# Kernel tuning notes

Hardware: AMD Instinct MI355X
Metric: run time of the kernel (lower is better)

Reference implementation:

```python
import jax, jax.numpy as jnp
import numpy as np

N = 65536        # nodes
E = 131072       # directed edges
D = 512          # emb_dim
L = 5            # num_layer
G = 512          # num graphs
EPS = 1e-5       # batchnorm eps
NUM_ATOM_TYPE, NUM_CHIRALITY = 120, 3
NUM_BOND_TYPE, NUM_BOND_DIR = 6, 3


def setup_inputs() -> dict:
    key = jax.random.key(0)
    ks = jax.random.split(key, 12)
    s = 0.02
    return {
        "x": jax.random.randint(ks[0], (N, 2), 0, 3),
        "edge_index": jax.random.randint(ks[1], (2, E), 0, N),
        "edge_attr": jax.random.randint(ks[2], (E, 2), 0, 3),
        "batch": jnp.sort(jax.random.randint(ks[3], (N,), 0, G)),
        "x_emb1": jax.random.normal(ks[4], (NUM_ATOM_TYPE, D), jnp.float32) * s,
        "x_emb2": jax.random.normal(ks[5], (NUM_CHIRALITY, D), jnp.float32) * s,
        "e_emb1": jax.random.normal(ks[6], (L, NUM_BOND_TYPE, D), jnp.float32) * s,
        "e_emb2": jax.random.normal(ks[7], (L, NUM_BOND_DIR, D), jnp.float32) * s,
        "W1": jax.random.normal(ks[8], (L, D, 2 * D), jnp.float32) * s,
        "b1": jnp.zeros((L, 2 * D), jnp.float32),
        "W2": jax.random.normal(ks[9], (L, 2 * D, D), jnp.float32) * s,
        "b2": jnp.zeros((L, D), jnp.float32),
        "gamma": jnp.ones((L, D), jnp.float32),
        "beta": jnp.zeros((L, D), jnp.float32),
    }


def reference(x, edge_index, edge_attr, batch,
              x_emb1, x_emb2, e_emb1, e_emb2,
              W1, b1, W2, b2, gamma, beta):
    n = x.shape[0]
    # atom embedding: type + chirality
    h = x_emb1[x[:, 0]] + x_emb2[x[:, 1]]                     # [N, D]

    # add self loops (appended after real edges, attr = [4, 0])
    loops = jnp.arange(n)
    src = jnp.concatenate([edge_index[0], loops])             # [E+N]
    dst = jnp.concatenate([edge_index[1], loops])
    sl_attr = jnp.concatenate(
        [jnp.full((n, 1), 4, dtype=edge_attr.dtype),
         jnp.zeros((n, 1), dtype=edge_attr.dtype)], axis=1)
    ea = jnp.concatenate([edge_attr, sl_attr], axis=0)        # [E+N, 2]

    for l in range(L):
        # per-edge embedding: bond type + bond direction
        e = e_emb1[l][ea[:, 0]] + e_emb2[l][ea[:, 1]]         # [E+N, D]
        msg = h[src] + e                                      # gather + add
        agg = jax.ops.segment_sum(msg, dst, num_segments=n)   # scatter-add
        # GIN MLP: Linear(D,2D) -> ReLU -> Linear(2D,D)
        hh = jax.nn.relu(agg @ W1[l] + b1[l]) @ W2[l] + b2[l]
        # BatchNorm1d (training-mode batch statistics)
        mean = hh.mean(axis=0)
        var = hh.var(axis=0)
        hh = (hh - mean) * jax.lax.rsqrt(var + EPS) * gamma[l] + beta[l]
        if l < L - 1:
            hh = jax.nn.relu(hh)   # dropout(p=0) is identity
        h = hh

    # JK='last': node rep = h; graph rep = global mean pool over batch ids
    counts = jax.ops.segment_sum(jnp.ones((n,), h.dtype), batch, num_segments=G)
    graph = jax.ops.segment_sum(h, batch, num_segments=G) / jnp.maximum(counts, 1.0)[:, None]
    return graph, h
```

## Files before the change

kernel.cpp:

```cpp
#include <hip/hip_runtime.h>
#include <stdint.h>

#define Nn 65536
#define Ee 131072
#define Dd 512
#define D2 1024
#define Ll 5
#define Gg 512
#define EPSf 1e-5f

typedef _Float16 f16x8 __attribute__((ext_vector_type(8)));
typedef float f32x4 __attribute__((ext_vector_type(4)));
typedef unsigned short u16x8 __attribute__((ext_vector_type(8)));

__device__ __forceinline__ unsigned short f2h(float f) {
    _Float16 h = (_Float16)f;
    union { _Float16 h; unsigned short u; } c; c.h = h;
    return c.u;
}

__device__ __forceinline__ float h2f(unsigned short s) {
    union { unsigned short s; _Float16 h; } c; c.s = s;
    return (float)c.h;
}

__device__ __forceinline__ void gload_lds16(const void* g, void* l) {
    __builtin_amdgcn_global_load_lds(
        (const __attribute__((address_space(1))) void*)(uintptr_t)g,
        (__attribute__((address_space(3))) void*)(unsigned)(uintptr_t)l,
        16, 0, 0);
}

__global__ void k_transW(const float* __restrict__ src, unsigned short* __restrict__ dst,
                         int K, int Nw) {
    long total = (long)Ll * K * Nw;
    for (long idx = (long)blockIdx.x * blockDim.x + threadIdx.x; idx < total;
         idx += (long)gridDim.x * blockDim.x) {
        long l = idx / ((long)K * Nw);
        long rem = idx - l * (long)K * Nw;
        int k = (int)(rem / Nw), n = (int)(rem % Nw);
        dst[(l * Nw + n) * K + k] = f2h(src[idx]);
    }
}

__global__ void k_etab(const float* __restrict__ ee1, const float* __restrict__ ee2,
                       float* __restrict__ E) {
    int idx = blockIdx.x * blockDim.x + threadIdx.x;
    const int total = Ll * 18 * Dd;
    if (idx < total) {
        int l = idx / (18 * Dd);
        int rem = idx - l * 18 * Dd;
        int j = rem / Dd, c = rem - j * Dd;
        int a0 = j / 3, a1 = j - a0 * 3;
        E[idx] = ee1[((size_t)l * 6 + a0) * Dd + c] + ee2[((size_t)l * 3 + a1) * Dd + c];
    }
}

__global__ void k_embed(const int* __restrict__ x,
                        const float* __restrict__ xe1, const float* __restrict__ xe2,
                        unsigned short* __restrict__ hhf) {
    const int total = Nn * 64;
    for (int idx = blockIdx.x * blockDim.x + threadIdx.x; idx < total;
         idx += gridDim.x * blockDim.x) {
        int node = idx >> 6, c8 = (idx & 63) * 8;
        int t0 = x[2 * node], t1 = x[2 * node + 1];
        const float4* p1 = (const float4*)(xe1 + (size_t)t0 * Dd + c8);
        const float4* p2 = (const float4*)(xe2 + (size_t)t1 * Dd + c8);
        float4 a0 = p1[0], a1 = p1[1], b0 = p2[0], b1 = p2[1];
        u16x8 o;
        o[0] = f2h(a0.x + b0.x); o[1] = f2h(a0.y + b0.y);
        o[2] = f2h(a0.z + b0.z); o[3] = f2h(a0.w + b0.w);
        o[4] = f2h(a1.x + b1.x); o[5] = f2h(a1.y + b1.y);
        o[6] = f2h(a1.z + b1.z); o[7] = f2h(a1.w + b1.w);
        *(u16x8*)(hhf + (size_t)node * Dd + c8) = o;
    }
}

__global__ void k_zeroN(int* __restrict__ p, int n) {
    int i = blockIdx.x * blockDim.x + threadIdx.x;
    if (i < n) p[i] = 0;
}

__global__ void k_hist(const int* __restrict__ edst, int* __restrict__ cnt) {
    int e = blockIdx.x * blockDim.x + threadIdx.x;
    if (e < Ee) atomicAdd(&cnt[edst[e]], 1);
}

__global__ void k_scan(const int* __restrict__ cnt, int* __restrict__ off,
                       int* __restrict__ cursor) {
    __shared__ int part[1024];
    int t = threadIdx.x;
    int base = t * 64;
    int s = 0;
    for (int i = 0; i < 64; ++i) s += cnt[base + i];
    part[t] = s;
    __syncthreads();
    for (int d = 1; d < 1024; d <<= 1) {
        int v = (t >= d) ? part[t - d] : 0;
        __syncthreads();
        part[t] += v;
        __syncthreads();
    }
    int run = part[t] - s;
    for (int i = 0; i < 64; ++i) {
        off[base + i] = run;
        cursor[base + i] = run;
        run += cnt[base + i];
    }
    if (t == 1023) off[Nn] = run;
}

__global__ void k_place(const int* __restrict__ esrc, const int* __restrict__ edst,
                        const int* __restrict__ eattr, int* __restrict__ cursor,
                        int* __restrict__ ckey, int* __restrict__ csrc) {
    int e = blockIdx.x * blockDim.x + threadIdx.x;
    if (e < Ee) {
        int d = edst[e];
        int p = atomicAdd(&cursor[d], 1);
        ckey[p] = e * 32 + (eattr[2 * e] * 3 + eattr[2 * e + 1]);
        csrc[p] = esrc[e];
    }
}

__global__ void k_sort(const int* __restrict__ off, int* __restrict__ ckey,
                       int* __restrict__ csrc) {
    int node = blockIdx.x * blockDim.x + threadIdx.x;
    if (node >= Nn) return;
    int kb = off[node], ke = off[node + 1];
    for (int i = kb + 1; i < ke; ++i) {
        int k = ckey[i], s = csrc[i];
        int j = i - 1;
        while (j >= kb && ckey[j] > k) {
            ckey[j + 1] = ckey[j]; csrc[j + 1] = csrc[j]; --j;
        }
        ckey[j + 1] = k; csrc[j + 1] = s;
    }
}

template <int NORM>
__global__ __launch_bounds__(256) void k_gather(const unsigned short* __restrict__ hf16,
                                                const float* __restrict__ ss,
                                                const int* __restrict__ off,
                                                const int* __restrict__ ckey,
                                                const int* __restrict__ csrc,
                                                const float* __restrict__ El,
                                                unsigned short* __restrict__ aggh) {
    int node = (blockIdx.x << 2) + (threadIdx.x >> 6);
    int lane = threadIdx.x & 63;
    int c8 = lane * 8;
    float sa[8], sb[8];
    if (NORM) {
        float4 a0 = *(const float4*)(ss + c8), a1 = *(const float4*)(ss + c8 + 4);
        float4 b0 = *(const float4*)(ss + 512 + c8), b1 = *(const float4*)(ss + 512 + c8 + 4);
        sa[0] = a0.x; sa[1] = a0.y; sa[2] = a0.z; sa[3] = a0.w;
        sa[4] = a1.x; sa[5] = a1.y; sa[6] = a1.z; sa[7] = a1.w;
        sb[0] = b0.x; sb[1] = b0.y; sb[2] = b0.z; sb[3] = b0.w;
        sb[4] = b1.x; sb[5] = b1.y; sb[6] = b1.z; sb[7] = b1.w;
    }
    float acc[8];
    {
        u16x8 v = *(const u16x8*)(hf16 + (size_t)node * Dd + c8);
        float4 e0 = *(const float4*)(El + 12 * Dd + c8);
        float4 e1 = *(const float4*)(El + 12 * Dd + c8 + 4);
        float ev[8];
        ev[0] = e0.x; ev[1] = e0.y; ev[2] = e0.z; ev[3] = e0.w;
        ev[4] = e1.x; ev[5] = e1.y; ev[6] = e1.z; ev[7] = e1.w;
#pragma unroll
        for (int i = 0; i < 8; ++i) {
            float hv = h2f(v[i]);
            if (NORM) hv = fmaxf(fmaf(hv, sa[i], sb[i]), 0.f);
            acc[i] = hv + ev[i];
        }
    }
    int kb = off[node], ke = off[node + 1];
    for (int k = kb; k < ke; ++k) {
        int src = csrc[k];
        int at = ckey[k] & 31;
        u16x8 v = *(const u16x8*)(hf16 + (size_t)src * Dd + c8);
        const float* Er = El + (size_t)at * Dd + c8;
        float4 e0 = *(const float4*)(Er);
        float4 e1 = *(const float4*)(Er + 4);
        float ev[8];
        ev[0] = e0.x; ev[1] = e0.y; ev[2] = e0.z; ev[3] = e0.w;
        ev[4] = e1.x; ev[5] = e1.y; ev[6] = e1.z; ev[7] = e1.w;
#pragma unroll
        for (int i = 0; i < 8; ++i) {
            float hv = h2f(v[i]);
            if (NORM) hv = fmaxf(fmaf(hv, sa[i], sb[i]), 0.f);
            acc[i] += hv + ev[i];
        }
    }
    u16x8 o;
#pragma unroll
    for (int i = 0; i < 8; ++i) o[i] = f2h(acc[i]);
    *(u16x8*)(aggh + (size_t)node * Dd + c8) = o;
}

__device__ __forceinline__ void stage_q(const unsigned short* __restrict__ g, int ldk,
                                        long row0, int col0, char* region, int tid) {
    int wbase = (tid >> 6) << 10;
#pragma unroll
    for (int r = 0; r < 2; ++r) {
        int gi = tid + r * 512;
        int row = gi >> 2;
        int k16 = (gi & 3) ^ ((row >> 1) & 3);
        gload_lds16(g + (row0 + row) * (long)ldk + col0 + k16 * 8,
                    region + r * 8192 + wbase);
    }
}

__device__ __forceinline__ f16x8 rd_frag(const char* region, int row, int l4) {
    int slot = l4 ^ ((row >> 1) & 3);
    return *(const f16x8*)(region + row * 64 + (slot << 4));
}

template <int EPI>
__global__ __launch_bounds__(512, 2) void gemm8(const unsigned short* __restrict__ A,
                                                const unsigned short* __restrict__ BT,
                                                const float* __restrict__ bias,
                                                unsigned short* __restrict__ Cb,
                                                float* __restrict__ pS,
                                                int M, int N, int K) {
    __shared__ __align__(16) char lds[131072];
    const int tid = threadIdx.x;
    const int lane = tid & 63;
    const int w = tid >> 6;
    const int wm = w >> 2, wn = w & 3;
    const int l15 = lane & 15, l4 = lane >> 4;

    const int nwg = gridDim.x;
    const int cpx = nwg >> 3;
    const int bid = blockIdx.x;
    const int wg = (bid & 7) * cpx + (bid >> 3);
    const int ntn = N >> 8;
    const long bm = (long)(wg / ntn) * 256;
    const long bn = (long)(wg % ntn) * 256;

    char* Ar = lds;
    char* Br = lds + 65536;
    const int NT = K >> 6;

    f32x4 acc[8][4];
#pragma unroll
    for (int i = 0; i < 8; ++i)
#pragma unroll
        for (int j = 0; j < 4; ++j) acc[i][j] = (f32x4){0.f, 0.f, 0.f, 0.f};

    stage_q(A, K, bm, 0, Ar, tid);
    stage_q(BT, K, bn, 0, Br, tid);
    stage_q(A, K, bm, 32, Ar + 16384, tid);
    stage_q(BT, K, bn, 32, Br + 16384, tid);
    asm volatile("s_waitcnt vmcnt(4)" ::: "memory");
    __builtin_amdgcn_s_barrier();
    asm volatile("" ::: "memory");

    for (int t = 0; t < NT; ++t) {
        const int par = (t & 1) << 15;
        const int npar = ((t + 1) & 1) << 15;
        const bool pre = (t + 1 < NT);
#pragma unroll
        for (int kh = 0; kh < 2; ++kh) {
            const char* Ac = Ar + par + kh * 16384;
            const char* Bc = Br + par + kh * 16384;
            f16x8 af[8], bv[4];
#pragma unroll
            for (int fn = 0; fn < 4; ++fn)
                bv[fn] = rd_frag(Bc, wn * 64 + fn * 16 + l15, l4);
#pragma unroll
            for (int fm = 0; fm < 8; ++fm)
                af[fm] = rd_frag(Ac, wm * 128 + fm * 16 + l15, l4);
            if (pre) {
                stage_q(BT, K, bn, (t + 1) * 64 + kh * 32, Br + npar + kh * 16384, tid);
                stage_q(A, K, bm, (t + 1) * 64 + kh * 32, Ar + npar + kh * 16384, tid);
            }
#pragma unroll
            for (int fm = 0; fm < 8; ++fm)
#pragma unroll
                for (int fn = 0; fn < 4; ++fn)
                    acc[fm][fn] = __builtin_amdgcn_mfma_f32_16x16x32_f16(af[fm], bv[fn], acc[fm][fn], 0, 0, 0);
            if (pre) {
                asm volatile("s_waitcnt vmcnt(4)" ::: "memory");
            } else {
                asm volatile("s_waitcnt vmcnt(0)" ::: "memory");
            }
            __builtin_amdgcn_s_barrier();
            asm volatile("" ::: "memory");
        }
    }

    unsigned short* cl = (unsigned short*)lds;
    float cs[4] = {0.f, 0.f, 0.f, 0.f}, cq[4] = {0.f, 0.f, 0.f, 0.f};
#pragma unroll
    for (int hh = 0; hh < 2; ++hh) {
        __syncthreads();
        if (wm == hh) {
#pragma unroll
            for (int fn = 0; fn < 4; ++fn) {
                int col = wn * 64 + fn * 16 + l15;
                float bval = bias[bn + col];
#pragma unroll
                for (int fm = 0; fm < 8; ++fm) {
                    int r0 = fm * 16 + l4 * 4;
#pragma unroll
                    for (int r = 0; r < 4; ++r) {
                        float v = acc[fm][fn][r] + bval;
                        if (EPI == 0) v = fmaxf(v, 0.f);
                        else { cs[fn] += v; cq[fn] += v * v; }
                        cl[(r0 + r) * 264 + col] = f2h(v);
                    }
                }
            }
        }
        __syncthreads();
#pragma unroll
        for (int i = 0; i < 8; ++i) {
            int g = tid + i * 512;
            int r = g >> 5, cg = (g & 31) << 3;
            u16x8 val = *(const u16x8*)&cl[r * 264 + cg];
            *(u16x8*)&Cb[(bm + hh * 128 + r) * N + bn + cg] = val;
        }
    }
    if (EPI == 1) {
#pragma unroll
        for (int fn = 0; fn < 4; ++fn) {
            float s = cs[fn], q = cq[fn];
            s += __shfl_xor(s, 16); s += __shfl_xor(s, 32);
            q += __shfl_xor(q, 16); q += __shfl_xor(q, 32);
            if (l4 == 0) {
                int col = (int)bn + wn * 64 + fn * 16 + l15;
                int rowgrp = ((int)(bm >> 8)) * 2 + wm;
                pS[rowgrp * 512 + col] = s;
                pS[262144 + rowgrp * 512 + col] = q;
            }
        }
    }
}

__global__ void k_bnA(const float* __restrict__ pS, float* __restrict__ pT) {
    int b = blockIdx.x;
    int t = threadIdx.x;
    float s0 = 0.f, s1 = 0.f, q0 = 0.f, q1 = 0.f;
#pragma unroll
    for (int i = 0; i < 8; ++i) {
        int rg = b * 8 + i;
        s0 += pS[rg * 512 + t];
        s1 += pS[rg * 512 + t + 256];
        q0 += pS[262144 + rg * 512 + t];
        q1 += pS[262144 + rg * 512 + t + 256];
    }
    pT[b * 512 + t] = s0;
    pT[b * 512 + t + 256] = s1;
    pT[32768 + b * 512 + t] = q0;
    pT[32768 + b * 512 + t + 256] = q1;
}

__global__ void k_bnB(const float* __restrict__ pT, const float* __restrict__ gamma,
                      const float* __restrict__ beta, float* __restrict__ ss) {
    int c = threadIdx.x;
    float s = 0.f, q = 0.f;
    for (int b = 0; b < 64; ++b) {
        s += pT[b * 512 + c];
        q += pT[32768 + b * 512 + c];
    }
    float mean = s * (1.f / (float)Nn);
    float var = q * (1.f / (float)Nn) - mean * mean;
    float a = gamma[c] * rsqrtf(var + EPSf);
    ss[c] = a;
    ss[512 + c] = beta[c] - mean * a;
}

__global__ void k_norm(const unsigned short* __restrict__ hhf, const float* __restrict__ ss,
                       float4* __restrict__ h4) {
    const int total = Nn * 128;
    const float4* ss4 = (const float4*)ss;
    for (int idx = blockIdx.x * blockDim.x + threadIdx.x; idx < total;
         idx += gridDim.x * blockDim.x) {
        int c = idx & 127;
        ushort4 u = *(const ushort4*)(hhf + (size_t)idx * 4);
        float4 v = make_float4(h2f(u.x), h2f(u.y), h2f(u.z), h2f(u.w));
        float4 a = ss4[c], b = ss4[128 + c];
        v.x = fmaf(v.x, a.x, b.x); v.y = fmaf(v.y, a.y, b.y);
        v.z = fmaf(v.z, a.z, b.z); v.w = fmaf(v.w, a.w, b.w);
        h4[idx] = v;
    }
}

__global__ void k_pool(const unsigned short* __restrict__ hhf, const float* __restrict__ ss,
                       const int* __restrict__ batch, float* __restrict__ graph) {
    int g = blockIdx.x, t = threadIdx.x;
    int lo = 0, hi = Nn;
    while (lo < hi) { int m = (lo + hi) >> 1; if (batch[m] < g) lo = m + 1; else hi = m; }
    int s = lo;
    lo = s; hi = Nn;
    while (lo < hi) { int m = (lo + hi) >> 1; if (batch[m] <= g) lo = m + 1; else hi = m; }
    int e = lo;
    float a0 = ss[t], a1 = ss[t + 256];
    float b0 = ss[512 + t], b1 = ss[512 + t + 256];
    float s0 = 0.f, s1 = 0.f;
    for (int r = s; r < e; ++r) {
        const unsigned short* row = hhf + (size_t)r * Dd;
        s0 += fmaf(h2f(row[t]), a0, b0);
        s1 += fmaf(h2f(row[t + 256]), a1, b1);
    }
    int cnt = e - s; if (cnt < 1) cnt = 1;
    float inv = 1.f / (float)cnt;
    graph[(long)g * Dd + t] = s0 * inv;
    graph[(long)g * Dd + t + 256] = s1 * inv;
}

extern "C" void kernel_launch(void* const* d_in, const int* in_sizes, int n_in,
                              void* d_out, int out_size, void* d_ws, size_t ws_size,
                              hipStream_t stream) {
    (void)in_sizes; (void)n_in; (void)out_size; (void)ws_size;
    const int* x      = (const int*)d_in[0];
    const int* ei     = (const int*)d_in[1];
    const int* ea     = (const int*)d_in[2];
    const int* batch  = (const int*)d_in[3];
    const float* xe1  = (const float*)d_in[4];
    const float* xe2  = (const float*)d_in[5];
    const float* ee1  = (const float*)d_in[6];
    const float* ee2  = (const float*)d_in[7];
    const float* W1   = (const float*)d_in[8];
    const float* b1   = (const float*)d_in[9];
    const float* W2   = (const float*)d_in[10];
    const float* b2   = (const float*)d_in[11];
    const float* gamma = (const float*)d_in[12];
    const float* beta  = (const float*)d_in[13];

    float* graph = (float*)d_out;
    float* h = graph + (size_t)Gg * Dd;

    char* w = (char*)d_ws;
    int* csr_off = (int*)w;                     w += (Nn + 1) * 4;
    int* cursor = (int*)w;                      w += Nn * 4;
    int* cnt = (int*)w;                         w += Nn * 4;
    int* ckey = (int*)w;                        w += Ee * 4;
    int* csrc = (int*)w;                        w += Ee * 4;
    float* ss = (float*)w;                      w += 4096;
    float* pS = (float*)w;                      w += 2 * 512 * 512 * 4;
    float* pT = (float*)w;                      w += 2 * 64 * 512 * 4;
    float* Etab = (float*)w;                    w += (size_t)Ll * 18 * Dd * 4;
    unsigned short* aggh = (unsigned short*)w;  w += (size_t)Nn * Dd * 2;
    unsigned short* hhf = (unsigned short*)w;   w += (size_t)Nn * Dd * 2;
    unsigned short* w1t = (unsigned short*)w;   w += (size_t)Ll * D2 * Dd * 2;
    unsigned short* w2t = (unsigned short*)w;   w += (size_t)Ll * Dd * D2 * 2;

    k_transW<<<2048, 256, 0, stream>>>(W1, w1t, Dd, D2);
    k_transW<<<2048, 256, 0, stream>>>(W2, w2t, D2, Dd);
    k_etab<<<(Ll * 18 * Dd + 255) / 256, 256, 0, stream>>>(ee1, ee2, Etab);
    k_embed<<<2048, 256, 0, stream>>>(x, xe1, xe2, hhf);

    k_zeroN<<<64, 1024, 0, stream>>>(cnt, Nn);
    k_hist<<<Ee / 256, 256, 0, stream>>>(ei + Ee, cnt);
    k_scan<<<1, 1024, 0, stream>>>(cnt, csr_off, cursor);
    k_place<<<Ee / 256, 256, 0, stream>>>(ei, ei + Ee, ea, cursor, ckey, csrc);
    k_sort<<<Nn / 256, 256, 0, stream>>>(csr_off, ckey, csrc);

    for (int l = 0; l < Ll; ++l) {
        const float* El = Etab + (size_t)l * 18 * Dd;
        if (l == 0)
            k_gather<0><<<Nn / 4, 256, 0, stream>>>(hhf, nullptr, csr_off, ckey, csrc,
                                                    El, aggh);
        else
            k_gather<1><<<Nn / 4, 256, 0, stream>>>(hhf, ss, csr_off, ckey, csrc,
                                                    El, aggh);
        gemm8<0><<<(Nn / 256) * (D2 / 256), 512, 0, stream>>>(
            aggh, w1t + (size_t)l * D2 * Dd, b1 + (size_t)l * D2,
            (unsigned short*)h, nullptr, Nn, D2, Dd);
        gemm8<1><<<(Nn / 256) * (Dd / 256), 512, 0, stream>>>(
            (const unsigned short*)h, w2t + (size_t)l * Dd * D2, b2 + (size_t)l * Dd,
            hhf, pS, Nn, Dd, D2);
        k_bnA<<<64, 256, 0, stream>>>(pS, pT);
        k_bnB<<<1, 512, 0, stream>>>(pT, gamma + (size_t)l * Dd, beta + (size_t)l * Dd, ss);
    }

    k_norm<<<2048, 256, 0, stream>>>(hhf, ss, (float4*)h);
    k_pool<<<Gg, 256, 0, stream>>>(hhf, ss, batch, graph);
}
```

Before: 1.433 ms.

## Load GEMM B fragments directly from global and deepen A-tile LDS pipeline

Restructures the MLP GEMM so that weight (B) fragments are read straight from global memory (likely L2-resident) into registers instead of being staged through LDS. The freed LDS is used for a 4-stage ring of A tiles prefetched three iterations ahead. The wave layout changes from 2x4 to 4x2, with each wave owning 64x128, and the BN partial-sum layout is widened to match. K becomes a template parameter. The risk is exposed global-load latency on B every iteration and higher register pressure from the larger per-wave fragment set.

Result: slower. 2.275 ms (+58.8%).

```diff
diff --git a/kernel.cpp b/kernel.cpp
--- a/kernel.cpp
+++ b/kernel.cpp
@@ -214,18 +214,18 @@
     return *(const f16x8*)(region + row * 64 + (slot << 4));
 }
 
-template <int EPI>
-__global__ __launch_bounds__(512, 2) void gemm8(const unsigned short* __restrict__ A,
-                                                const unsigned short* __restrict__ BT,
-                                                const float* __restrict__ bias,
-                                                unsigned short* __restrict__ Cb,
-                                                float* __restrict__ pS,
-                                                int M, int N, int K) {
+template <int EPI, int KK>
+__global__ __launch_bounds__(512, 2) void gemm_bd(const unsigned short* __restrict__ A,
+                                                  const unsigned short* __restrict__ BT,
+                                                  const float* __restrict__ bias,
+                                                  unsigned short* __restrict__ Cb,
+                                                  float* __restrict__ pS,
+                                                  int M, int N) {
     __shared__ __align__(16) char lds[131072];
     const int tid = threadIdx.x;
     const int lane = tid & 63;
     const int w = tid >> 6;
-    const int wm = w >> 2, wn = w & 3;
+    const int wm = w >> 1, wn = w & 1;
     const int l15 = lane & 15, l4 = lane >> 4;
 
     const int nwg = gridDim.x;
@@ -236,70 +236,82 @@
     const long bm = (long)(wg / ntn) * 256;
     const long bn = (long)(wg % ntn) * 256;
 
-    char* Ar = lds;
-    char* Br = lds + 65536;
-    const int NT = K >> 6;
-
-    f32x4 acc[8][4];
-#pragma unroll
-    for (int i = 0; i < 8; ++i)
-#pragma unroll
-        for (int j = 0; j < 4; ++j) acc[i][j] = (f32x4){0.f, 0.f, 0.f, 0.f};
-
-    stage_q(A, K, bm, 0, Ar, tid);
-    stage_q(BT, K, bn, 0, Br, tid);
-    stage_q(A, K, bm, 32, Ar + 16384, tid);
-    stage_q(BT, K, bn, 32, Br + 16384, tid);
-    asm volatile("s_waitcnt vmcnt(4)" ::: "memory");
+    const int NT = KK >> 6;
+
+    const unsigned short* Bl = BT + (size_t)(bn + wn * 128 + l15) * KK + l4 * 8;
+
+    f32x4 acc[4][8];
+#pragma unroll
+    for (int i = 0; i < 4; ++i)
+#pragma unroll
+        for (int j = 0; j < 8; ++j) acc[i][j] = (f32x4){0.f, 0.f, 0.f, 0.f};
+
+    stage_q(A, KK, bm, 0, lds, tid);
+    stage_q(A, KK, bm, 32, lds + 16384, tid);
+    stage_q(A, KK, bm, 64, lds + 32768, tid);
+    stage_q(A, KK, bm, 96, lds + 32768 + 16384, tid);
+    stage_q(A, KK, bm, 128, lds + 65536, tid);
+    stage_q(A, KK, bm, 160, lds + 65536 + 16384, tid);
+    asm volatile("s_waitcnt vmcnt(8)" ::: "memory");
     __builtin_amdgcn_s_barrier();
     asm volatile("" ::: "memory");
 
     for (int t = 0; t < NT; ++t) {
-        const int par = (t & 1) << 15;
-        const int npar = ((t + 1) & 1) << 15;
-        const bool pre = (t + 1 < NT);
-#pragma unroll
-        for (int kh = 0; kh < 2; ++kh) {
-            const char* Ac = Ar + par + kh * 16384;
-            const char* Bc = Br + par + kh * 16384;
-            f16x8 af[8], bv[4];
-#pragma unroll
-            for (int fn = 0; fn < 4; ++fn)
-                bv[fn] = rd_frag(Bc, wn * 64 + fn * 16 + l15, l4);
-#pragma unroll
-            for (int fm = 0; fm < 8; ++fm)
-                af[fm] = rd_frag(Ac, wm * 128 + fm * 16 + l15, l4);
-            if (pre) {
-                stage_q(BT, K, bn, (t + 1) * 64 + kh * 32, Br + npar + kh * 16384, tid);
-                stage_q(A, K, bm, (t + 1) * 64 + kh * 32, Ar + npar + kh * 16384, tid);
-            }
-#pragma unroll
-            for (int fm = 0; fm < 8; ++fm)
-#pragma unroll
-                for (int fn = 0; fn < 4; ++fn)
-                    acc[fm][fn] = __builtin_amdgcn_mfma_f32_16x16x32_f16(af[fm], bv[fn], acc[fm][fn], 0, 0, 0);
-            if (pre) {
-                asm volatile("s_waitcnt vmcnt(4)" ::: "memory");
-            } else {
-                asm volatile("s_waitcnt vmcnt(0)" ::: "memory");
-            }
-            __builtin_amdgcn_s_barrier();
-            asm volatile("" ::: "memory");
-        }
+        const char* Ac = lds + (size_t)(t & 3) * 32768;
+        const unsigned short* Bt = Bl + t * 64;
+        f16x8 af0[4], af1[4], bv0[8], bv1[8];
+#pragma unroll
+        for (int fn = 0; fn < 8; ++fn)
+            bv0[fn] = *(const f16x8*)(Bt + (size_t)fn * 16 * KK);
+#pragma unroll
+        for (int fn = 0; fn < 8; ++fn)
+            bv1[fn] = *(const f16x8*)(Bt + (size_t)fn * 16 * KK + 32);
+#pragma unroll
+        for (int fm = 0; fm < 4; ++fm)
+            af0[fm] = rd_frag(Ac, wm * 64 + fm * 16 + l15, l4);
+#pragma unroll
+        for (int fm = 0; fm < 4; ++fm)
+            af1[fm] = rd_frag(Ac + 16384, wm * 64 + fm * 16 + l15, l4);
+        if (t + 3 < NT) {
+            char* dst = lds + (size_t)((t + 3) & 3) * 32768;
+            stage_q(A, KK, bm, (t + 3) * 64, dst, tid);
+            stage_q(A, KK, bm, (t + 3) * 64 + 32, dst + 16384, tid);
+        }
+#pragma unroll
+        for (int fm = 0; fm < 4; ++fm)
+#pragma unroll
+            for (int fn = 0; fn < 8; ++fn)
+                acc[fm][fn] = __builtin_amdgcn_mfma_f32_16x16x32_f16(af0[fm], bv0[fn], acc[fm][fn], 0, 0, 0);
+#pragma unroll
+        for (int fm = 0; fm < 4; ++fm)
+#pragma unroll
+            for (int fn = 0; fn < 8; ++fn)
+                acc[fm][fn] = __builtin_amdgcn_mfma_f32_16x16x32_f16(af1[fm], bv1[fn], acc[fm][fn], 0, 0, 0);
+        if (t + 3 < NT) {
+            asm volatile("s_waitcnt vmcnt(8)" ::: "memory");
+        } else if (t + 2 < NT) {
+            asm volatile("s_waitcnt vmcnt(4)" ::: "memory");
+        } else if (t + 1 < NT) {
+            asm volatile("s_waitcnt vmcnt(0)" ::: "memory");
+        }
+        __builtin_amdgcn_s_barrier();
+        asm volatile("" ::: "memory");
     }
 
     unsigned short* cl = (unsigned short*)lds;
-    float cs[4] = {0.f, 0.f, 0.f, 0.f}, cq[4] = {0.f, 0.f, 0.f, 0.f};
-#pragma unroll
-    for (int hh = 0; hh < 2; ++hh) {
+    float cs[8], cq[8];
+#pragma unroll
+    for (int i = 0; i < 8; ++i) { cs[i] = 0.f; cq[i] = 0.f; }
+#pragma unroll
+    for (int q = 0; q < 4; ++q) {
         __syncthreads();
-        if (wm == hh) {
-#pragma unroll
-            for (int fn = 0; fn < 4; ++fn) {
-                int col = wn * 64 + fn * 16 + l15;
+        if (wm == q) {
+#pragma unroll
+            for (int fn = 0; fn < 8; ++fn) {
+                int col = wn * 128 + fn * 16 + l15;
                 float bval = bias[bn + col];
 #pragma unroll
-                for (int fm = 0; fm < 8; ++fm) {
+                for (int fm = 0; fm < 4; ++fm) {
                     int r0 = fm * 16 + l4 * 4;
 #pragma unroll
                     for (int r = 0; r < 4; ++r) {
@@ -313,24 +325,24 @@
         }
         __syncthreads();
 #pragma unroll
-        for (int i = 0; i < 8; ++i) {
+        for (int i = 0; i < 4; ++i) {
             int g = tid + i * 512;
             int r = g >> 5, cg = (g & 31) << 3;
             u16x8 val = *(const u16x8*)&cl[r * 264 + cg];
-            *(u16x8*)&Cb[(bm + hh * 128 + r) * N + bn + cg] = val;
+            *(u16x8*)&Cb[(bm + q * 64 + r) * N + bn + cg] = val;
         }
     }
     if (EPI == 1) {
 #pragma unroll
-        for (int fn = 0; fn < 4; ++fn) {
+        for (int fn = 0; fn < 8; ++fn) {
             float s = cs[fn], q = cq[fn];
             s += __shfl_xor(s, 16); s += __shfl_xor(s, 32);
             q += __shfl_xor(q, 16); q += __shfl_xor(q, 32);
             if (l4 == 0) {
-                int col = (int)bn + wn * 64 + fn * 16 + l15;
-                int rowgrp = ((int)(bm >> 8)) * 2 + wm;
+                int col = (int)bn + wn * 128 + fn * 16 + l15;
+                int rowgrp = (int)(bm >> 6) + wm;
                 pS[rowgrp * 512 + col] = s;
-                pS[262144 + rowgrp * 512 + col] = q;
+                pS[524288 + rowgrp * 512 + col] = q;
             }
         }
     }
@@ -341,12 +353,12 @@
     int t = threadIdx.x;
     float s0 = 0.f, s1 = 0.f, q0 = 0.f, q1 = 0.f;
 #pragma unroll
-    for (int i = 0; i < 8; ++i) {
-        int rg = b * 8 + i;
+    for (int i = 0; i < 16; ++i) {
+        int rg = b * 16 + i;
         s0 += pS[rg * 512 + t];
         s1 += pS[rg * 512 + t + 256];
-        q0 += pS[262144 + rg * 512 + t];
-        q1 += pS[262144 + rg * 512 + t + 256];
+        q0 += pS[524288 + rg * 512 + t];
+        q1 += pS[524288 + rg * 512 + t + 256];
     }
     pT[b * 512 + t] = s0;
     pT[b * 512 + t + 256] = s1;
@@ -437,7 +449,7 @@
     int* ckey = (int*)w;                        w += Ee * 4;
     int* csrc = (int*)w;                        w += Ee * 4;
     float* ss = (float*)w;                      w += 4096;
-    float* pS = (float*)w;                      w += 2 * 512 * 512 * 4;
+    float* pS = (float*)w;                      w += 2 * 1024 * 512 * 4;
     float* pT = (float*)w;                      w += 2 * 64 * 512 * 4;
     float* Etab = (float*)w;                    w += (size_t)Ll * 18 * Dd * 4;
     unsigned short* aggh = (unsigned short*)w;  w += (size_t)Nn * Dd * 2;
@@ -464,12 +476,12 @@
         else
             k_gather<1><<<Nn / 4, 256, 0, stream>>>(hhf, ss, csr_off, ckey, csrc,
                                                     El, aggh);
-        gemm8<0><<<(Nn / 256) * (D2 / 256), 512, 0, stream>>>(
+        gemm_bd<0, Dd><<<(Nn / 256) * (D2 / 256), 512, 0, stream>>>(
             aggh, w1t + (size_t)l * D2 * Dd, b1 + (size_t)l * D2,
-            (unsigned short*)h, nullptr, Nn, D2, Dd);
-        gemm8<1><<<(Nn / 256) * (Dd / 256), 512, 0, stream>>>(
+            (unsigned short*)h, nullptr, Nn, D2);
+        gemm_bd<1, D2><<<(Nn / 256) * (Dd / 256), 512, 0, stream>>>(
             (const unsigned short*)h, w2t + (size_t)l * Dd * D2, b2 + (size_t)l * Dd,
-            hhf, pS, Nn, Dd, D2);
+            hhf, pS, Nn, Dd);
         k_bnA<<<64, 256, 0, stream>>>(pS, pT);
         k_bnB<<<1, 512, 0, stream>>>(pT, gamma + (size_t)l * Dd, beta + (size_t)l * Dd, ss);
     }
```

## Restructure GEMM to 4 waves with 128x128 warp tiles and 3-stage LDS pipeline

Applied to the files above, without the earlier changes.

The 256x256 GEMM tile is now computed by 4 waves instead of 8, so each wave owns a 128x128 sub-tile with an 8x8 accumulator array, which raises MFMA work per LDS fragment read. The K loop now steps 32 at a time through a triple-buffered LDS ring that prefetches two stages ahead, replacing the old double-buffered 64-wide steps. The epilogue is split into four 64-row passes. The trade-off is much higher register pressure (256 accumulator floats per lane), one workgroup per CU, and fewer waves to hide latency.

New measurement: 1.567 ms. +9.3%, slower.

```diff
diff --git a/kernel.cpp b/kernel.cpp
--- a/kernel.cpp
+++ b/kernel.cpp
@@ -196,16 +196,16 @@
     *(u16x8*)(aggh + (size_t)node * Dd + c8) = o;
 }
 
-__device__ __forceinline__ void stage_q(const unsigned short* __restrict__ g, int ldk,
+__device__ __forceinline__ void stage_r(const unsigned short* __restrict__ g, int ldk,
                                         long row0, int col0, char* region, int tid) {
     int wbase = (tid >> 6) << 10;
 #pragma unroll
-    for (int r = 0; r < 2; ++r) {
-        int gi = tid + r * 512;
+    for (int r = 0; r < 4; ++r) {
+        int gi = tid + r * 256;
         int row = gi >> 2;
         int k16 = (gi & 3) ^ ((row >> 1) & 3);
         gload_lds16(g + (row0 + row) * (long)ldk + col0 + k16 * 8,
-                    region + r * 8192 + wbase);
+                    region + r * 4096 + wbase);
     }
 }
 
@@ -215,17 +215,17 @@
 }
 
 template <int EPI>
-__global__ __launch_bounds__(512, 2) void gemm8(const unsigned short* __restrict__ A,
-                                                const unsigned short* __restrict__ BT,
-                                                const float* __restrict__ bias,
-                                                unsigned short* __restrict__ Cb,
-                                                float* __restrict__ pS,
-                                                int M, int N, int K) {
-    __shared__ __align__(16) char lds[131072];
+__global__ __launch_bounds__(256, 1) void gemm_bt(const unsigned short* __restrict__ A,
+                                                  const unsigned short* __restrict__ BT,
+                                                  const float* __restrict__ bias,
+                                                  unsigned short* __restrict__ Cb,
+                                                  float* __restrict__ pS,
+                                                  int M, int N, int K) {
+    __shared__ __align__(16) char lds[98304];
     const int tid = threadIdx.x;
     const int lane = tid & 63;
     const int w = tid >> 6;
-    const int wm = w >> 2, wn = w & 3;
+    const int wm = w >> 1, wn = w & 1;
     const int l15 = lane & 15, l4 = lane >> 4;
 
     const int nwg = gridDim.x;
@@ -236,77 +236,76 @@
     const long bm = (long)(wg / ntn) * 256;
     const long bn = (long)(wg % ntn) * 256;
 
-    char* Ar = lds;
-    char* Br = lds + 65536;
-    const int NT = K >> 6;
-
-    f32x4 acc[8][4];
+    const int NT = K >> 5;
+
+    f32x4 acc[8][8];
 #pragma unroll
     for (int i = 0; i < 8; ++i)
 #pragma unroll
-        for (int j = 0; j < 4; ++j) acc[i][j] = (f32x4){0.f, 0.f, 0.f, 0.f};
-
-    stage_q(A, K, bm, 0, Ar, tid);
-    stage_q(BT, K, bn, 0, Br, tid);
-    stage_q(A, K, bm, 32, Ar + 16384, tid);
-    stage_q(BT, K, bn, 32, Br + 16384, tid);
-    asm volatile("s_waitcnt vmcnt(4)" ::: "memory");
+        for (int j = 0; j < 8; ++j) acc[i][j] = (f32x4){0.f, 0.f, 0.f, 0.f};
+
+    stage_r(A, K, bm, 0, lds, tid);
+    stage_r(BT, K, bn, 0, lds + 16384, tid);
+    stage_r(A, K, bm, 32, lds + 32768, tid);
+    stage_r(BT, K, bn, 32, lds + 32768 + 16384, tid);
+    asm volatile("s_waitcnt vmcnt(8)" ::: "memory");
     __builtin_amdgcn_s_barrier();
     asm volatile("" ::: "memory");
 
+    int cur = 0, nx2 = 2;
     for (int t = 0; t < NT; ++t) {
-        const int par = (t & 1) << 15;
-        const int npar = ((t + 1) & 1) << 15;
-        const bool pre = (t + 1 < NT);
-#pragma unroll
-        for (int kh = 0; kh < 2; ++kh) {
-            const char* Ac = Ar + par + kh * 16384;
-            const char* Bc = Br + par + kh * 16384;
-            f16x8 af[8], bv[4];
-#pragma unroll
-            for (int fn = 0; fn < 4; ++fn)
-                bv[fn] = rd_frag(Bc, wn * 64 + fn * 16 + l15, l4);
-#pragma unroll
-            for (int fm = 0; fm < 8; ++fm)
-                af[fm] = rd_frag(Ac, wm * 128 + fm * 16 + l15, l4);
-            if (pre) {
-                stage_q(BT, K, bn, (t + 1) * 64 + kh * 32, Br + npar + kh * 16384, tid);
-                stage_q(A, K, bm, (t + 1) * 64 + kh * 32, Ar + npar + kh * 16384, tid);
-            }
-#pragma unroll
-            for (int fm = 0; fm < 8; ++fm)
-#pragma unroll
-                for (int fn = 0; fn < 4; ++fn)
-                    acc[fm][fn] = __builtin_amdgcn_mfma_f32_16x16x32_f16(af[fm], bv[fn], acc[fm][fn], 0, 0, 0);
-            if (pre) {
-                asm volatile("s_waitcnt vmcnt(4)" ::: "memory");
-            } else {
-                asm volatile("s_waitcnt vmcnt(0)" ::: "memory");
-            }
-            __builtin_amdgcn_s_barrier();
-            asm volatile("" ::: "memory");
-        }
+        const char* Ac = lds + cur * 32768;
+        const char* Bc = Ac + 16384;
+        f16x8 af[8], bv[8];
+#pragma unroll
+        for (int fn = 0; fn < 8; ++fn)
+            bv[fn] = rd_frag(Bc, wn * 128 + fn * 16 + l15, l4);
+#pragma unroll
+        for (int fm = 0; fm < 8; ++fm)
+            af[fm] = rd_frag(Ac, wm * 128 + fm * 16 + l15, l4);
+        if (t + 2 < NT) {
+            char* dst = lds + nx2 * 32768;
+            stage_r(A, K, bm, (t + 2) * 32, dst, tid);
+            stage_r(BT, K, bn, (t + 2) * 32, dst + 16384, tid);
+        }
+#pragma unroll
+        for (int fm = 0; fm < 8; ++fm)
+#pragma unroll
+            for (int fn = 0; fn < 8; ++fn)
+                acc[fm][fn] = __builtin_amdgcn_mfma_f32_16x16x32_f16(af[fm], bv[fn], acc[fm][fn], 0, 0, 0);
+        if (t + 2 < NT) {
+            asm volatile("s_waitcnt vmcnt(8)" ::: "memory");
+        } else if (t + 1 < NT) {
+            asm volatile("s_waitcnt vmcnt(0)" ::: "memory");
+        }
+        __builtin_amdgcn_s_barrier();
+        asm volatile("" ::: "memory");
+        cur = (cur == 2) ? 0 : cur + 1;
+        nx2 = (nx2 == 2) ? 0 : nx2 + 1;
     }
 
     unsigned short* cl = (unsigned short*)lds;
-    float cs[4] = {0.f, 0.f, 0.f, 0.f}, cq[4] = {0.f, 0.f, 0.f, 0.f};
-#pragma unroll
-    for (int hh = 0; hh < 2; ++hh) {
+    float cs[8], cq[8];
+#pragma unroll
+    for (int i = 0; i < 8; ++i) { cs[i] = 0.f; cq[i] = 0.f; }
+#pragma unroll
+    for (int q = 0; q < 4; ++q) {
         __syncthreads();
-        if (wm == hh) {
-#pragma unroll
-            for (int fn = 0; fn < 4; ++fn) {
-                int col = wn * 64 + fn * 16 + l15;
+        if (wm == (q >> 1)) {
+#pragma unroll
+            for (int fn = 0; fn < 8; ++fn) {
+                int col = wn * 128 + fn * 16 + l15;
                 float bval = bias[bn + col];
 #pragma unroll
-                for (int fm = 0; fm < 8; ++fm) {
-                    int r0 = fm * 16 + l4 * 4;
+                for (int fi = 0; fi < 4; ++fi) {
+                    const int fm = (q & 1) * 4 + fi;
+                    int rl = fi * 16 + l4 * 4;
 #pragma unroll
                     for (int r = 0; r < 4; ++r) {
                         float v = acc[fm][fn][r] + bval;
                         if (EPI == 0) v = fmaxf(v, 0.f);
                         else { cs[fn] += v; cq[fn] += v * v; }
-                        cl[(r0 + r) * 264 + col] = f2h(v);
+                        cl[(rl + r) * 264 + col] = f2h(v);
                     }
                 }
             }
@@ -314,20 +313,20 @@
         __syncthreads();
 #pragma unroll
         for (int i = 0; i < 8; ++i) {
-            int g = tid + i * 512;
+            int g = tid + i * 256;
             int r = g >> 5, cg = (g & 31) << 3;
             u16x8 val = *(const u16x8*)&cl[r * 264 + cg];
-            *(u16x8*)&Cb[(bm + hh * 128 + r) * N + bn + cg] = val;
+            *(u16x8*)&Cb[(bm + q * 64 + r) * N + bn + cg] = val;
         }
     }
     if (EPI == 1) {
 #pragma unroll
-        for (int fn = 0; fn < 4; ++fn) {
+        for (int fn = 0; fn < 8; ++fn) {
             float s = cs[fn], q = cq[fn];
             s += __shfl_xor(s, 16); s += __shfl_xor(s, 32);
             q += __shfl_xor(q, 16); q += __shfl_xor(q, 32);
             if (l4 == 0) {
-                int col = (int)bn + wn * 64 + fn * 16 + l15;
+                int col = (int)bn + wn * 128 + fn * 16 + l15;
                 int rowgrp = ((int)(bm >> 8)) * 2 + wm;
                 pS[rowgrp * 512 + col] = s;
                 pS[262144 + rowgrp * 512 + col] = q;
@@ -464,10 +463,10 @@
         else
             k_gather<1><<<Nn / 4, 256, 0, stream>>>(hhf, ss, csr_off, ckey, csrc,
                                                     El, aggh);
-        gemm8<0><<<(Nn / 256) * (D2 / 256), 512, 0, stream>>>(
+        gemm_bt<0><<<(Nn / 256) * (D2 / 256), 256, 0, stream>>>(
             aggh, w1t + (size_t)l * D2 * Dd, b1 + (size_t)l * D2,
             (unsigned short*)h, nullptr, Nn, D2, Dd);
-        gemm8<1><<<(Nn / 256) * (Dd / 256), 512, 0, stream>>>(
+        gemm_bt<1><<<(Nn / 256) * (Dd / 256), 256, 0, stream>>>(
             (const unsigned short*)h, w2t + (size_t)l * Dd * D2, b2 + (size_t)l * Dd,
             hhf, pS, Nn, Dd, D2);
         k_bnA<<<64, 256, 0, stream>>>(pS, pT);
```

## Restructure GEMM K-loop into four-stage LDS ring with three tiles in flight

Applied to the files above, without the earlier changes.

Replaces the double-buffered 64-wide K-step pipeline with a 4-slot ring of 32-wide K tiles in LDS, prefetching three tiles ahead. The aim is to hide more global-load latency behind MFMA work. In exchange there is one barrier per 32-wide K step, with no extra LDS use. The vmcnt waits are tuned to the number of outstanding stages.

Measured after the change: 1.437 ms. Within noise of the previous version (+0.2%).

```diff
diff --git a/kernel.cpp b/kernel.cpp
--- a/kernel.cpp
+++ b/kernel.cpp
@@ -196,7 +196,7 @@
     *(u16x8*)(aggh + (size_t)node * Dd + c8) = o;
 }
 
-__device__ __forceinline__ void stage_q(const unsigned short* __restrict__ g, int ldk,
+__device__ __forceinline__ void stage_h(const unsigned short* __restrict__ g, int ldk,
                                         long row0, int col0, char* region, int tid) {
     int wbase = (tid >> 6) << 10;
 #pragma unroll
@@ -215,12 +215,12 @@
 }
 
 template <int EPI>
-__global__ __launch_bounds__(512, 2) void gemm8(const unsigned short* __restrict__ A,
-                                                const unsigned short* __restrict__ BT,
-                                                const float* __restrict__ bias,
-                                                unsigned short* __restrict__ Cb,
-                                                float* __restrict__ pS,
-                                                int M, int N, int K) {
+__global__ __launch_bounds__(512, 2) void gemm_dp(const unsigned short* __restrict__ A,
+                                                  const unsigned short* __restrict__ BT,
+                                                  const float* __restrict__ bias,
+                                                  unsigned short* __restrict__ Cb,
+                                                  float* __restrict__ pS,
+                                                  int M, int N, int K) {
     __shared__ __align__(16) char lds[131072];
     const int tid = threadIdx.x;
     const int lane = tid & 63;
@@ -236,9 +236,7 @@
     const long bm = (long)(wg / ntn) * 256;
     const long bn = (long)(wg % ntn) * 256;
 
-    char* Ar = lds;
-    char* Br = lds + 65536;
-    const int NT = K >> 6;
+    const int NT = K >> 5;
 
     f32x4 acc[8][4];
 #pragma unroll
@@ -246,46 +244,45 @@
 #pragma unroll
         for (int j = 0; j < 4; ++j) acc[i][j] = (f32x4){0.f, 0.f, 0.f, 0.f};
 
-    stage_q(A, K, bm, 0, Ar, tid);
-    stage_q(BT, K, bn, 0, Br, tid);
-    stage_q(A, K, bm, 32, Ar + 16384, tid);
-    stage_q(BT, K, bn, 32, Br + 16384, tid);
-    asm volatile("s_waitcnt vmcnt(4)" ::: "memory");
+    stage_h(A, K, bm, 0, lds, tid);
+    stage_h(BT, K, bn, 0, lds + 16384, tid);
+    stage_h(A, K, bm, 32, lds + 32768, tid);
+    stage_h(BT, K, bn, 32, lds + 32768 + 16384, tid);
+    stage_h(A, K, bm, 64, lds + 65536, tid);
+    stage_h(BT, K, bn, 64, lds + 65536 + 16384, tid);
+    asm volatile("s_waitcnt vmcnt(8)" ::: "memory");
     __builtin_amdgcn_s_barrier();
     asm volatile("" ::: "memory");
 
     for (int t = 0; t < NT; ++t) {
-        const int par = (t & 1) << 15;
-        const int npar = ((t + 1) & 1) << 15;
-        const bool pre = (t + 1 < NT);
-#pragma unroll
-        for (int kh = 0; kh < 2; ++kh) {
-            const char* Ac = Ar + par + kh * 16384;
-            const char* Bc = Br + par + kh * 16384;
-            f16x8 af[8], bv[4];
+        const char* Ac = lds + (size_t)(t & 3) * 32768;
+        const char* Bc = Ac + 16384;
+        f16x8 af[8], bv[4];
+#pragma unroll
+        for (int fn = 0; fn < 4; ++fn)
+            bv[fn] = rd_frag(Bc, wn * 64 + fn * 16 + l15, l4);
+#pragma unroll
+        for (int fm = 0; fm < 8; ++fm)
+            af[fm] = rd_frag(Ac, wm * 128 + fm * 16 + l15, l4);
+        if (t + 3 < NT) {
+            char* dst = lds + (size_t)((t + 3) & 3) * 32768;
+            stage_h(A, K, bm, (t + 3) * 32, dst, tid);
+            stage_h(BT, K, bn, (t + 3) * 32, dst + 16384, tid);
+        }
+#pragma unroll
+        for (int fm = 0; fm < 8; ++fm)
 #pragma unroll
             for (int fn = 0; fn < 4; ++fn)
-                bv[fn] = rd_frag(Bc, wn * 64 + fn * 16 + l15, l4);
-#pragma unroll
-            for (int fm = 0; fm < 8; ++fm)
-                af[fm] = rd_frag(Ac, wm * 128 + fm * 16 + l15, l4);
-            if (pre) {
-                stage_q(BT, K, bn, (t + 1) * 64 + kh * 32, Br + npar + kh * 16384, tid);
-                stage_q(A, K, bm, (t + 1) * 64 + kh * 32, Ar + npar + kh * 16384, tid);
-            }
-#pragma unroll
-            for (int fm = 0; fm < 8; ++fm)
-#pragma unroll
-                for (int fn = 0; fn < 4; ++fn)
-                    acc[fm][fn] = __builtin_amdgcn_mfma_f32_16x16x32_f16(af[fm], bv[fn], acc[fm][fn], 0, 0, 0);
-            if (pre) {
-                asm volatile("s_waitcnt vmcnt(4)" ::: "memory");
-            } else {
-                asm volatile("s_waitcnt vmcnt(0)" ::: "memory");
-            }
-            __builtin_amdgcn_s_barrier();
-            asm volatile("" ::: "memory");
-        }
+                acc[fm][fn] = __builtin_amdgcn_mfma_f32_16x16x32_f16(af[fm], bv[fn], acc[fm][fn], 0, 0, 0);
+        if (t + 3 < NT) {
+            asm volatile("s_waitcnt vmcnt(8)" ::: "memory");
+        } else if (t + 2 < NT) {
+            asm volatile("s_waitcnt vmcnt(4)" ::: "memory");
+        } else if (t + 1 < NT) {
+            asm volatile("s_waitcnt vmcnt(0)" ::: "memory");
+        }
+        __builtin_amdgcn_s_barrier();
+        asm volatile("" ::: "memory");
     }
 
     unsigned short* cl = (unsigned short*)lds;
@@ -464,10 +461,10 @@
         else
             k_gather<1><<<Nn / 4, 256, 0, stream>>>(hhf, ss, csr_off, ckey, csrc,
                                                     El, aggh);
-        gemm8<0><<<(Nn / 256) * (D2 / 256), 512, 0, stream>>>(
+        gemm_dp<0><<<(Nn / 256) * (D2 / 256), 512, 0, stream>>>(
             aggh, w1t + (size_t)l * D2 * Dd, b1 + (size_t)l * D2,
             (unsigned short*)h, nullptr, Nn, D2, Dd);
-        gemm8<1><<<(Nn / 256) * (Dd / 256), 512, 0, stream>>>(
+        gemm_dp<1><<<(Nn / 256) * (Dd / 256), 512, 0, stream>>>(
             (const unsigned short*)h, w2t + (size_t)l * Dd * D2, b2 + (size_t)l * Dd,
             hhf, pS, Nn, Dd, D2);
         k_bnA<<<64, 256, 0, stream>>>(pS, pT);
```
